# Performance work log

Hardware: AMD Instinct MI355X
Metric: run time of the kernel (lower is better)

## Reference

```python
import jax, jax.numpy as jnp
import numpy as np
from jax import lax

MAX_SCALE = 4
SCALES = [2 ** i for i in range(1, MAX_SCALE + 1)]  # [2, 4, 8, 16]
EPS = 1e-6
BN_EPS = 1e-3  # keras BatchNormalization default epsilon


def _box_sum(x, r):
    # DepthwiseConv2D with ones kernel, SAME zero padding == box sum window
    return lax.reduce_window(x, 0.0, lax.add, (1, r, r, 1), (1, 1, 1, 1), 'SAME')


def setup_inputs() -> dict:
    key = jax.random.key(0)
    k1, k2 = jax.random.split(key)
    B, H, W, C, K = 4, 224, 224, 64, 8
    return {
        'x': jax.random.normal(k1, (B, H, W, C), dtype=jnp.float32),
        'ols_weights': jnp.ones((MAX_SCALE,), jnp.float32),
        'anchors': jax.random.normal(k2, (C, K), dtype=jnp.float32),
        'hist_widths': jnp.ones((C, K), jnp.float32),
        'bn_gamma': jnp.ones((C,), jnp.float32),
        'bn_beta': jnp.zeros((C,), jnp.float32),
        'bn_mean': jnp.zeros((C,), jnp.float32),
        'bn_var': jnp.ones((C,), jnp.float32),
    }


def reference(x, ols_weights, anchors, hist_widths, bn_gamma, bn_beta, bn_mean, bn_var):
    # --- sample min-max scaling to [0, 1] per sample ---
    xmin = jnp.min(x, axis=(1, 2, 3), keepdims=True)
    xmax = jnp.max(x, axis=(1, 2, 3), keepdims=True)
    xs = (x - xmin) / (xmax - xmin + EPS)

    # --- multi-scale box measures: [B,H,W,C,S] ---
    measures = jnp.stack([_box_sum(xs, r) for r in SCALES], axis=-1)

    # --- weighted OLS slope of log(measure) vs log(scale) -> local alpha ---
    ly = jnp.log(measures + EPS)                         # [B,H,W,C,S]
    lr = jnp.log(jnp.asarray(SCALES, jnp.float32))       # [S]
    w = ols_weights                                       # [S]
    wsum = jnp.sum(w)
    lr_bar = jnp.sum(w * lr) / wsum
    ly_bar = jnp.sum(w * ly, axis=-1, keepdims=True) / wsum
    dx = lr - lr_bar                                      # [S]
    num = jnp.sum(w * dx * (ly - ly_bar), axis=-1)        # [B,H,W,C]
    den = jnp.sum(w * dx * dx)
    alphas = num / den

    # --- batch norm (inference mode, training=False) ---
    a = bn_gamma * (alphas - bn_mean) * lax.rsqrt(bn_var + BN_EPS) + bn_beta

    # --- triangular soft histogram over k anchors, relu'd and summed ---
    hist = 1.0 - hist_widths * jnp.abs(a[..., None] - anchors)  # [B,H,W,C,K]
    soft_counts = jnp.sum(jax.nn.relu(hist), axis=-1)           # [B,H,W,C]

    return x + jax.nn.sigmoid(soft_counts)
```

## Files before the change

kernel.cpp:

```cpp
#include <hip/hip_runtime.h>
#include <math.h>

#define B 4
#define H 224
#define W 224
#define C 64
#define K 8
#define WC (W*C)
#define HWC (H*W*C)

__device__ inline float wave_reduce_min(float v) {
  #pragma unroll
  for (int off = 32; off > 0; off >>= 1)
    v = fminf(v, __shfl_down(v, off, 64));
  return v;
}
__device__ inline float wave_reduce_max(float v) {
  #pragma unroll
  for (int off = 32; off > 0; off >>= 1)
    v = fmaxf(v, __shfl_down(v, off, 64));
  return v;
}

__global__ __launch_bounds__(256) void k_minmax_part(const float* __restrict__ x,
                                                     float* __restrict__ scratch) {
  int s   = blockIdx.x >> 9;
  int blk = blockIdx.x & 511;
  const float4* xs = (const float4*)(x + (size_t)s * HWC);
  const int n4 = HWC / 4;
  float vmin = INFINITY, vmax = -INFINITY;
  for (int i = blk*256 + threadIdx.x; i < n4; i += 512*256) {
    float4 v = xs[i];
    vmin = fminf(vmin, fminf(fminf(v.x, v.y), fminf(v.z, v.w)));
    vmax = fmaxf(vmax, fmaxf(fmaxf(v.x, v.y), fmaxf(v.z, v.w)));
  }
  __shared__ float smin[4], smax[4];
  float wmin = wave_reduce_min(vmin), wmax = wave_reduce_max(vmax);
  int wave = threadIdx.x >> 6, lane = threadIdx.x & 63;
  if (lane == 0) { smin[wave] = wmin; smax[wave] = wmax; }
  __syncthreads();
  if (threadIdx.x == 0) {
    float m = fminf(fminf(smin[0], smin[1]), fminf(smin[2], smin[3]));
    float M = fmaxf(fmaxf(smax[0], smax[1]), fmaxf(smax[2], smax[3]));
    scratch[blockIdx.x]        = m;
    scratch[2048 + blockIdx.x] = M;
  }
}

__global__ __launch_bounds__(256) void k_vpfx(const float* __restrict__ x,
                                              const float* __restrict__ scratch,
                                              float* __restrict__ P) {
  int bid = blockIdx.x;
  int b = bid / W, w = bid % W;
  int q = threadIdx.x >> 6, c = threadIdx.x & 63;

  float vmin = fminf(scratch[b*512 + threadIdx.x], scratch[b*512 + 256 + threadIdx.x] - 0.f);
  float vmax = fmaxf(scratch[2048 + b*512 + threadIdx.x], scratch[2048 + b*512 + 256 + threadIdx.x]);
  __shared__ float smin[4], smax[4];
  float wmin = wave_reduce_min(vmin), wmax = wave_reduce_max(vmax);
  if ((threadIdx.x & 63) == 0) { smin[q] = wmin; smax[q] = wmax; }
  __syncthreads();
  float xmin = fminf(fminf(smin[0], smin[1]), fminf(smin[2], smin[3]));
  float xmax = fmaxf(fmaxf(smax[0], smax[1]), fmaxf(smax[2], smax[3]));
  float inv  = 1.0f / (xmax - xmin + 1e-6f);

  size_t colbase = (size_t)b*HWC + (size_t)w*C + c;
  const int hq = q * 56;
  const float* xp = x + colbase + (size_t)hq * WC;

  float v[56];
  #pragma unroll
  for (int j = 0; j < 56; ++j) v[j] = xp[(size_t)j * WC];
  float sum = 0.f;
  #pragma unroll
  for (int j = 0; j < 56; ++j) sum += v[j];

  __shared__ float lds[256];
  lds[threadIdx.x] = sum;
  __syncthreads();

  float acc = 0.f;
  for (int qq = 0; qq < q; ++qq) acc += lds[qq*64 + c];

  float* Pp = P + colbase + (size_t)hq * WC;
  #pragma unroll
  for (int j = 0; j < 56; ++j) {
    acc += v[j];
    Pp[(size_t)j * WC] = (acc - (float)(hq + j + 1) * xmin) * inv;
  }
}

__global__ __launch_bounds__(128) void k_main(
    const float* __restrict__ P, const float* __restrict__ x,
    const float* __restrict__ ols, const float* __restrict__ anchors,
    const float* __restrict__ hwidths, const float* __restrict__ bn_gamma,
    const float* __restrict__ bn_beta, const float* __restrict__ bn_mean,
    const float* __restrict__ bn_var, float* __restrict__ out) {
  int xcd  = blockIdx.x & 7;
  int i    = blockIdx.x >> 3;
  int rg   = xcd * 112 + (i >> 2);
  int wave = threadIdx.x >> 6, c = threadIdx.x & 63;
  int chunk = (i & 3) * 2 + wave;
  int b = rg / H, h = rg % H;
  int w0 = chunk * 28;

  const float LN2 = 0.69314718055994530942f;
  float wg0 = ols[0], wg1 = ols[1], wg2 = ols[2], wg3 = ols[3];
  float l0 = LN2, l1 = 2.f*LN2, l2 = 3.f*LN2, l3 = 4.f*LN2;
  float wsum = wg0 + wg1 + wg2 + wg3;
  float lrbar = (wg0*l0 + wg1*l1 + wg2*l2 + wg3*l3) / wsum;
  float d0 = l0-lrbar, d1 = l1-lrbar, d2 = l2-lrbar, d3 = l3-lrbar;
  float den = wg0*d0*d0 + wg1*d1*d1 + wg2*d2*d2 + wg3*d3*d3;
  float c0 = wg0*d0/den, c1 = wg1*d1/den, c2 = wg2*d2/den, c3 = wg3*d3/den;

  float scl  = bn_gamma[c] * rsqrtf(bn_var[c] + 1e-3f);
  float bofs = bn_beta[c] - bn_mean[c] * scl;
  float anc[K], wd[K];
  #pragma unroll
  for (int k = 0; k < K; ++k) { anc[k] = anchors[c*K + k]; wd[k] = hwidths[c*K + k]; }

  const int hiA[4] = {1, 2, 4, 8};
  const int loA[4] = {0, 1, 3, 7};
  const float* pt[4]; const float* pb[4]; float fb[4];
  #pragma unroll
  for (int s = 0; s < 4; ++s) {
    int ht = h + hiA[s]; if (ht > H-1) ht = H-1;
    int hb = h - loA[s] - 1;
    int hbc = hb < 0 ? 0 : hb;
    pt[s] = P + (size_t)b*HWC + (size_t)ht*WC + c;
    pb[s] = P + (size_t)b*HWC + (size_t)hbc*WC + c;
    fb[s] = hb < 0 ? 0.f : 1.f;
  }

  const float* xrow = x   + (size_t)b*HWC + (size_t)h*WC + c;
  float*       orow = out + (size_t)b*HWC + (size_t)h*WC + c;

  float ring2[2]   = {0,0};
  float ring4[4]   = {0,0,0,0};
  float ring8[8]   = {0,0,0,0,0,0,0,0};
  float ring16[16] = {0,0,0,0,0,0,0,0,0,0,0,0,0,0,0,0};
  float T0 = 0.f, T1 = 0.f, T2 = 0.f, T3 = 0.f;
  float abuf[8] = {0,0,0,0,0,0,0,0};

  for (int t0 = 0; t0 < 48; t0 += 16) {
    #pragma unroll
    for (int u = 0; u < 16; ++u) {
      int t  = t0 + u;
      int wr = w0 - 7 + t;
      float m0 = 0.f, m1 = 0.f, m2 = 0.f, m3 = 0.f;
      if (wr >= 0 && wr < W) {
        int off = wr * C;
        m0 = pt[0][off] - fb[0]*pb[0][off];
        m1 = pt[1][off] - fb[1]*pb[1][off];
        m2 = pt[2][off] - fb[2]*pb[2][off];
        m3 = pt[3][off] - fb[3]*pb[3][off];
      }
      T0 += m0 - ring2[u&1];  ring2[u&1]  = m0;
      T1 += m1 - ring4[u&3];  ring4[u&3]  = m1;
      T2 += m2 - ring8[u&7];  ring8[u&7]  = m2;
      T3 += m3 - ring16[u];   ring16[u]   = m3;
      abuf[(u+7)&7] += c0 * __logf(fmaxf(T0, 0.f) + 1e-6f);
      abuf[(u+6)&7] += c1 * __logf(fmaxf(T1, 0.f) + 1e-6f);
      abuf[(u+4)&7] += c2 * __logf(fmaxf(T2, 0.f) + 1e-6f);
      abuf[u&7]     += c3 * __logf(fmaxf(T3, 0.f) + 1e-6f);
      int ig = w0 - 15 + t;
      if (t >= 15 && ig <= w0 + 27) {
        float alpha = abuf[u&7];
        float a = alpha * scl + bofs;
        float sc = 0.f;
        #pragma unroll
        for (int k = 0; k < K; ++k)
          sc += fmaxf(0.f, 1.f - wd[k]*fabsf(a - anc[k]));
        float sig = 1.f / (1.f + __expf(-sc));
        float xv = __builtin_nontemporal_load(&xrow[ig*C]);
        __builtin_nontemporal_store(xv + sig, &orow[ig*C]);
      }
      abuf[u&7] = 0.f;
    }
  }
}

extern "C" void kernel_launch(void* const* d_in, const int* in_sizes, int n_in,
                              void* d_out, int out_size, void* d_ws, size_t ws_size,
                              hipStream_t stream) {
  const float* x        = (const float*)d_in[0];
  const float* ols      = (const float*)d_in[1];
  const float* anchors  = (const float*)d_in[2];
  const float* hwidths  = (const float*)d_in[3];
  const float* bn_gamma = (const float*)d_in[4];
  const float* bn_beta  = (const float*)d_in[5];
  const float* bn_mean  = (const float*)d_in[6];
  const float* bn_var   = (const float*)d_in[7];
  float* out = (float*)d_out;
  float* P   = (float*)d_ws;
  float* scratch = out;

  hipLaunchKernelGGL(k_minmax_part, dim3(2048),  dim3(256), 0, stream, x, scratch);
  hipLaunchKernelGGL(k_vpfx,        dim3(B*W),   dim3(256), 0, stream, x, scratch, P);
  hipLaunchKernelGGL(k_main,        dim3(B*H*4), dim3(128), 0, stream,
                     P, x, ols, anchors, hwidths, bn_gamma, bn_beta, bn_mean, bn_var, out);
}
```

Before: 215.0 us.

## Fold min-max normalization into box sums and drop separate min-max pass

The prefix-sum kernel now stores raw column prefix sums and emits per-column min/max partials, which removes the standalone min-max reduction pass over x. The main kernel reduces those partials itself and applies the normalization algebraically: it subtracts count*xmin from the raw box sums and scales the epsilon by the range, since a log slope is invariant to a constant scale. Interior tiles get a specialized loop with no bounds checks and precomputed constants. The trade-off is an extra small reduction in every main-kernel block, plus a dependence on enough workspace for the partials, with a fallback to the old path otherwise.

```diff
diff --git a/kernel.cpp b/kernel.cpp
--- a/kernel.cpp
+++ b/kernel.cpp
@@ -21,6 +21,199 @@
     v = fmaxf(v, __shfl_down(v, off, 64));
   return v;
 }
+
+struct FalseT { static constexpr bool value = false; };
+struct TrueT  { static constexpr bool value = true; };
+
+
+__global__ __launch_bounds__(256) void k_vpfx_raw(const float* __restrict__ x,
+                                                  float* __restrict__ P,
+                                                  float* __restrict__ pmin,
+                                                  float* __restrict__ pmax) {
+  int bid = blockIdx.x;
+  int b = bid / W, w = bid % W;
+  int q = threadIdx.x >> 6, c = threadIdx.x & 63;
+  size_t colbase = (size_t)b*HWC + (size_t)w*C + c;
+  const int hq = q * 56;
+  const float* xp = x + colbase + (size_t)hq * WC;
+
+  float v[56];
+  #pragma unroll
+  for (int j = 0; j < 56; ++j) v[j] = xp[(size_t)j * WC];
+
+  float sum = 0.f, vmin = v[0], vmax = v[0];
+  #pragma unroll
+  for (int j = 0; j < 56; ++j) {
+    sum += v[j];
+    vmin = fminf(vmin, v[j]);
+    vmax = fmaxf(vmax, v[j]);
+  }
+
+  __shared__ float lds[256];
+  __shared__ float smin[4], smax[4];
+  lds[threadIdx.x] = sum;
+  float wmin = wave_reduce_min(vmin), wmax = wave_reduce_max(vmax);
+  if ((threadIdx.x & 63) == 0) { smin[q] = wmin; smax[q] = wmax; }
+  __syncthreads();
+  if (threadIdx.x == 0) {
+    pmin[bid] = fminf(fminf(smin[0], smin[1]), fminf(smin[2], smin[3]));
+    pmax[bid] = fmaxf(fmaxf(smax[0], smax[1]), fmaxf(smax[2], smax[3]));
+  }
+
+  float acc = 0.f;
+  for (int qq = 0; qq < q; ++qq) acc += lds[qq*64 + c];
+
+  float* Pp = P + colbase + (size_t)hq * WC;
+  #pragma unroll
+  for (int j = 0; j < 56; ++j) {
+    acc += v[j];
+    Pp[(size_t)j * WC] = acc;
+  }
+}
+
+__global__ __launch_bounds__(128) void k_main2(
+    const float* __restrict__ P, const float* __restrict__ x,
+    const float* __restrict__ pmin, const float* __restrict__ pmax,
+    const float* __restrict__ ols, const float* __restrict__ anchors,
+    const float* __restrict__ hwidths, const float* __restrict__ bn_gamma,
+    const float* __restrict__ bn_beta, const float* __restrict__ bn_mean,
+    const float* __restrict__ bn_var, float* __restrict__ out) {
+  int xcd  = blockIdx.x & 7;
+  int i    = blockIdx.x >> 3;
+  int rg   = xcd * 112 + (i >> 2);
+  int wave = threadIdx.x >> 6, c = threadIdx.x & 63;
+  int chunk = (i & 3) * 2 + wave;
+  int b = rg / H, h = rg % H;
+  int w0 = chunk * 28;
+
+  float vmin = INFINITY, vmax = -INFINITY;
+  for (int ii = threadIdx.x; ii < W; ii += 128) {
+    vmin = fminf(vmin, pmin[b*W + ii]);
+    vmax = fmaxf(vmax, pmax[b*W + ii]);
+  }
+  vmin = wave_reduce_min(vmin);
+  vmax = wave_reduce_max(vmax);
+  __shared__ float sred[4];
+  if ((threadIdx.x & 63) == 0) { sred[wave*2] = vmin; sred[wave*2+1] = vmax; }
+  __syncthreads();
+  float xmin = fminf(sred[0], sred[2]);
+  float xmax = fmaxf(sred[1], sred[3]);
+  float rng  = xmax - xmin + 1e-6f;
+  float epsp = 1e-6f * rng;
+
+  const float LN2 = 0.69314718055994530942f;
+  float wg0 = ols[0], wg1 = ols[1], wg2 = ols[2], wg3 = ols[3];
+  float l0 = LN2, l1 = 2.f*LN2, l2 = 3.f*LN2, l3 = 4.f*LN2;
+  float wsum = wg0 + wg1 + wg2 + wg3;
+  float lrbar = (wg0*l0 + wg1*l1 + wg2*l2 + wg3*l3) / wsum;
+  float d0 = l0-lrbar, d1 = l1-lrbar, d2 = l2-lrbar, d3 = l3-lrbar;
+  float den = wg0*d0*d0 + wg1*d1*d1 + wg2*d2*d2 + wg3*d3*d3;
+  float c0 = wg0*d0/den, c1 = wg1*d1/den, c2 = wg2*d2/den, c3 = wg3*d3/den;
+
+  float scl  = bn_gamma[c] * rsqrtf(bn_var[c] + 1e-3f);
+  float bofs = bn_beta[c] - bn_mean[c] * scl;
+  float anc[K], wd[K];
+  #pragma unroll
+  for (int k = 0; k < K; ++k) { anc[k] = anchors[c*K + k]; wd[k] = hwidths[c*K + k]; }
+
+  const int hiA[4] = {1, 2, 4, 8};
+  const int loA[4] = {0, 1, 3, 7};
+  const int rA[4]  = {2, 4, 8, 16};
+  const float* pt[4]; const float* pb[4]; float fb[4];
+  float Anh[4], Kin[4];
+  #pragma unroll
+  for (int s = 0; s < 4; ++s) {
+    int ht = h + hiA[s]; if (ht > H-1) ht = H-1;
+    int hb = h - loA[s] - 1;
+    int hbc = hb < 0 ? 0 : hb;
+    pt[s] = P + (size_t)b*HWC + (size_t)ht*WC + c;
+    pb[s] = P + (size_t)b*HWC + (size_t)hbc*WC + c;
+    fb[s] = hb < 0 ? 0.f : 1.f;
+    int h0 = h - loA[s]; if (h0 < 0) h0 = 0;
+    int nv = ht - h0 + 1;
+    Anh[s] = -(float)nv * xmin;
+    Kin[s] = (float)rA[s] * Anh[s] + epsp;
+  }
+
+  const float* xrow = x   + (size_t)b*HWC + (size_t)h*WC + c;
+  float*       orow = out + (size_t)b*HWC + (size_t)h*WC + c;
+
+  auto tloop = [&](auto EDGEC) {
+    constexpr bool EDGE = decltype(EDGEC)::value;
+    float ring2[2]   = {0,0};
+    float ring4[4]   = {0,0,0,0};
+    float ring8[8]   = {0,0,0,0,0,0,0,0};
+    float ring16[16] = {0,0,0,0,0,0,0,0,0,0,0,0,0,0,0,0};
+    float T0 = 0.f, T1 = 0.f, T2 = 0.f, T3 = 0.f;
+    float abuf[8] = {0,0,0,0,0,0,0,0};
+
+    for (int t0 = 0; t0 < 48; t0 += 16) {
+      #pragma unroll
+      for (int u = 0; u < 16; ++u) {
+        int t  = t0 + u;
+        int wr = w0 - 7 + t;
+        float m0, m1, m2, m3;
+        if constexpr (EDGE) {
+          m0 = m1 = m2 = m3 = 0.f;
+          if (wr >= 0 && wr < W) {
+            int off = wr * C;
+            m0 = pt[0][off] - fb[0]*pb[0][off];
+            m1 = pt[1][off] - fb[1]*pb[1][off];
+            m2 = pt[2][off] - fb[2]*pb[2][off];
+            m3 = pt[3][off] - fb[3]*pb[3][off];
+          }
+        } else {
+          int off = wr * C;
+          m0 = pt[0][off] - fb[0]*pb[0][off];
+          m1 = pt[1][off] - fb[1]*pb[1][off];
+          m2 = pt[2][off] - fb[2]*pb[2][off];
+          m3 = pt[3][off] - fb[3]*pb[3][off];
+        }
+        T0 += m0 - ring2[u&1];  ring2[u&1]  = m0;
+        T1 += m1 - ring4[u&3];  ring4[u&3]  = m1;
+        T2 += m2 - ring8[u&7];  ring8[u&7]  = m2;
+        T3 += m3 - ring16[u];   ring16[u]   = m3;
+
+        float a0, a1, a2, a3;
+        if constexpr (EDGE) {
+          float nh0 = (float)(min(wr, W-1) - max(wr-1,  0) + 1);
+          float nh1 = (float)(min(wr, W-1) - max(wr-3,  0) + 1);
+          float nh2 = (float)(min(wr, W-1) - max(wr-7,  0) + 1);
+          float nh3 = (float)(min(wr, W-1) - max(wr-15, 0) + 1);
+          a0 = fmaxf(fmaf(Anh[0], nh0, T0) + epsp, epsp);
+          a1 = fmaxf(fmaf(Anh[1], nh1, T1) + epsp, epsp);
+          a2 = fmaxf(fmaf(Anh[2], nh2, T2) + epsp, epsp);
+          a3 = fmaxf(fmaf(Anh[3], nh3, T3) + epsp, epsp);
+        } else {
+          a0 = fmaxf(T0 + Kin[0], epsp);
+          a1 = fmaxf(T1 + Kin[1], epsp);
+          a2 = fmaxf(T2 + Kin[2], epsp);
+          a3 = fmaxf(T3 + Kin[3], epsp);
+        }
+        abuf[(u+7)&7] += c0 * __logf(a0);
+        abuf[(u+6)&7] += c1 * __logf(a1);
+        abuf[(u+4)&7] += c2 * __logf(a2);
+        abuf[u&7]     += c3 * __logf(a3);
+
+        int ig = w0 - 15 + t;
+        if (t >= 15 && ig <= w0 + 27) {
+          float alpha = abuf[u&7];
+          float a = alpha * scl + bofs;
+          float sc = 0.f;
+          #pragma unroll
+          for (int k = 0; k < K; ++k)
+            sc += fmaxf(0.f, 1.f - wd[k]*fabsf(a - anc[k]));
+          float sig = 1.f / (1.f + __expf(-sc));
+          float xv = __builtin_nontemporal_load(&xrow[ig*C]);
+          __builtin_nontemporal_store(xv + sig, &orow[ig*C]);
+        }
+        abuf[u&7] = 0.f;
+      }
+    }
+  };
+  if (w0 >= 22 && w0 <= 183) tloop(FalseT{}); else tloop(TrueT{});
+}
+
 
 __global__ __launch_bounds__(256) void k_minmax_part(const float* __restrict__ x,
                                                      float* __restrict__ scratch) {
@@ -180,6 +373,7 @@
   }
 }
 
+
 extern "C" void kernel_launch(void* const* d_in, const int* in_sizes, int n_in,
                               void* d_out, int out_size, void* d_ws, size_t ws_size,
                               hipStream_t stream) {
@@ -193,10 +387,21 @@
   const float* bn_var   = (const float*)d_in[7];
   float* out = (float*)d_out;
   float* P   = (float*)d_ws;
-  float* scratch = out;
-
-  hipLaunchKernelGGL(k_minmax_part, dim3(2048),  dim3(256), 0, stream, x, scratch);
-  hipLaunchKernelGGL(k_vpfx,        dim3(B*W),   dim3(256), 0, stream, x, scratch, P);
-  hipLaunchKernelGGL(k_main,        dim3(B*H*4), dim3(128), 0, stream,
-                     P, x, ols, anchors, hwidths, bn_gamma, bn_beta, bn_mean, bn_var, out);
-}
+  const size_t PBYTES = (size_t)B * HWC * sizeof(float);
+
+  if (ws_size >= PBYTES + 8192) {
+    float* pmn = (float*)((char*)d_ws + PBYTES);
+    float* pmx = pmn + 1024;
+    hipLaunchKernelGGL(k_vpfx_raw, dim3(B*W),   dim3(256), 0, stream, x, P, pmn, pmx);
+    hipLaunchKernelGGL(k_main2,    dim3(B*H*4), dim3(128), 0, stream,
+                       P, x, pmn, pmx, ols, anchors, hwidths,
+                       bn_gamma, bn_beta, bn_mean, bn_var, out);
+  } else {
+    float* scratch = out;
+    hipLaunchKernelGGL(k_minmax_part, dim3(2048),  dim3(256), 0, stream, x, scratch);
+    hipLaunchKernelGGL(k_vpfx,        dim3(B*W),   dim3(256), 0, stream, x, scratch, P);
+    hipLaunchKernelGGL(k_main,        dim3(B*H*4), dim3(128), 0, stream,
+                       P, x, ols, anchors, hwidths,
+                       bn_gamma, bn_beta, bn_mean, bn_var, out);
+  }
+}
```

Result: slower. 227.4 us (+5.8%).

## Fuse min-max reduction into column prefix kernel using cooperative grid sync

Applied to the files above, without the earlier changes.

Replaces the separate min/max pass and the column prefix-sum kernel with one cooperative kernel. It loads each column once into registers with float4 vectors, computes the partial min/max and segment sums, then runs a grid-wide sync before normalising and writing P. This removes a full extra read of x and one kernel launch. The cost is a grid barrier, which needs all 896 blocks to be resident at once (launch bounds 256,4). If the cooperative launch fails or the workspace is too small, it falls back to the old three-kernel path.

```diff
diff --git a/kernel.cpp b/kernel.cpp
--- a/kernel.cpp
+++ b/kernel.cpp
@@ -1,4 +1,5 @@
 #include <hip/hip_runtime.h>
+#include <hip/hip_cooperative_groups.h>
 #include <math.h>
 
 #define B 4
@@ -9,6 +10,8 @@
 #define WC (W*C)
 #define HWC (H*W*C)
 
+namespace cg = cooperative_groups;
+
 __device__ inline float wave_reduce_min(float v) {
   #pragma unroll
   for (int off = 32; off > 0; off >>= 1)
@@ -22,71 +25,89 @@
   return v;
 }
 
-__global__ __launch_bounds__(256) void k_minmax_part(const float* __restrict__ x,
-                                                     float* __restrict__ scratch) {
-  int s   = blockIdx.x >> 9;
-  int blk = blockIdx.x & 511;
-  const float4* xs = (const float4*)(x + (size_t)s * HWC);
-  const int n4 = HWC / 4;
-  float vmin = INFINITY, vmax = -INFINITY;
-  for (int i = blk*256 + threadIdx.x; i < n4; i += 512*256) {
-    float4 v = xs[i];
-    vmin = fminf(vmin, fminf(fminf(v.x, v.y), fminf(v.z, v.w)));
-    vmax = fmaxf(vmax, fmaxf(fmaxf(v.x, v.y), fmaxf(v.z, v.w)));
-  }
-  __shared__ float smin[4], smax[4];
-  float wmin = wave_reduce_min(vmin), wmax = wave_reduce_max(vmax);
-  int wave = threadIdx.x >> 6, lane = threadIdx.x & 63;
-  if (lane == 0) { smin[wave] = wmin; smax[wave] = wmax; }
-  __syncthreads();
-  if (threadIdx.x == 0) {
-    float m = fminf(fminf(smin[0], smin[1]), fminf(smin[2], smin[3]));
-    float M = fmaxf(fmaxf(smax[0], smax[1]), fmaxf(smax[2], smax[3]));
-    scratch[blockIdx.x]        = m;
-    scratch[2048 + blockIdx.x] = M;
-  }
-}
-
-__global__ __launch_bounds__(256) void k_vpfx(const float* __restrict__ x,
-                                              const float* __restrict__ scratch,
-                                              float* __restrict__ P) {
+
+__global__ __launch_bounds__(256, 4) void k_vpfx_coop(const float* __restrict__ x,
+                                                      float* __restrict__ P,
+                                                      float* __restrict__ pmin,
+                                                      float* __restrict__ pmax) {
+  cg::grid_group grid = cg::this_grid();
+
   int bid = blockIdx.x;
   int b = bid / W, w = bid % W;
-  int q = threadIdx.x >> 6, c = threadIdx.x & 63;
-
-  float vmin = fminf(scratch[b*512 + threadIdx.x], scratch[b*512 + 256 + threadIdx.x] - 0.f);
-  float vmax = fmaxf(scratch[2048 + b*512 + threadIdx.x], scratch[2048 + b*512 + 256 + threadIdx.x]);
+  int seg = threadIdx.x >> 4;
+  int chg = threadIdx.x & 15;
+
+  const size_t colbase = (size_t)b*HWC + (size_t)w*C;
+  const float4* xp4 = (const float4*)(x + colbase);
+  const int RS4 = WC / 4;
+  const int r0 = seg * 14;
+
+  float4 v4[14];
+  #pragma unroll
+  for (int j = 0; j < 14; ++j) v4[j] = xp4[(size_t)(r0 + j) * RS4 + chg];
+
+  float4 s4 = v4[0];
+  float vmin = fminf(fminf(v4[0].x, v4[0].y), fminf(v4[0].z, v4[0].w));
+  float vmax = fmaxf(fmaxf(v4[0].x, v4[0].y), fmaxf(v4[0].z, v4[0].w));
+  #pragma unroll
+  for (int j = 1; j < 14; ++j) {
+    s4.x += v4[j].x; s4.y += v4[j].y; s4.z += v4[j].z; s4.w += v4[j].w;
+    vmin = fminf(vmin, fminf(fminf(v4[j].x, v4[j].y), fminf(v4[j].z, v4[j].w)));
+    vmax = fmaxf(vmax, fmaxf(fmaxf(v4[j].x, v4[j].y), fmaxf(v4[j].z, v4[j].w)));
+  }
+
+  __shared__ float4 segsum[16][16];
   __shared__ float smin[4], smax[4];
-  float wmin = wave_reduce_min(vmin), wmax = wave_reduce_max(vmax);
-  if ((threadIdx.x & 63) == 0) { smin[q] = wmin; smax[q] = wmax; }
+  segsum[seg][chg] = s4;
+  float wmn = wave_reduce_min(vmin), wmx = wave_reduce_max(vmax);
+  int wv = threadIdx.x >> 6;
+  if ((threadIdx.x & 63) == 0) { smin[wv] = wmn; smax[wv] = wmx; }
+  __syncthreads();
+
+  if (threadIdx.x == 0) {
+    pmin[bid] = fminf(fminf(smin[0], smin[1]), fminf(smin[2], smin[3]));
+    pmax[bid] = fmaxf(fmaxf(smax[0], smax[1]), fmaxf(smax[2], smax[3]));
+  }
+
+  float4 o4 = {0.f, 0.f, 0.f, 0.f};
+  #pragma unroll
+  for (int ss = 0; ss < 16; ++ss) {
+    if (ss < seg) {
+      float4 t = segsum[ss][chg];
+      o4.x += t.x; o4.y += t.y; o4.z += t.z; o4.w += t.w;
+    }
+  }
+
+  __threadfence();
+  grid.sync();
+
+  float fmn = INFINITY, fmx = -INFINITY;
+  for (int ii = b*W + (int)threadIdx.x; ii < b*W + W; ii += 256) {
+    fmn = fminf(fmn, pmin[ii]);
+    fmx = fmaxf(fmx, pmax[ii]);
+  }
+  fmn = wave_reduce_min(fmn);
+  fmx = wave_reduce_max(fmx);
+  __syncthreads();
+  if ((threadIdx.x & 63) == 0) { smin[wv] = fmn; smax[wv] = fmx; }
   __syncthreads();
   float xmin = fminf(fminf(smin[0], smin[1]), fminf(smin[2], smin[3]));
   float xmax = fmaxf(fmaxf(smax[0], smax[1]), fmaxf(smax[2], smax[3]));
   float inv  = 1.0f / (xmax - xmin + 1e-6f);
 
-  size_t colbase = (size_t)b*HWC + (size_t)w*C + c;
-  const int hq = q * 56;
-  const float* xp = x + colbase + (size_t)hq * WC;
-
-  float v[56];
-  #pragma unroll
-  for (int j = 0; j < 56; ++j) v[j] = xp[(size_t)j * WC];
-  float sum = 0.f;
-  #pragma unroll
-  for (int j = 0; j < 56; ++j) sum += v[j];
-
-  __shared__ float lds[256];
-  lds[threadIdx.x] = sum;
-  __syncthreads();
-
-  float acc = 0.f;
-  for (int qq = 0; qq < q; ++qq) acc += lds[qq*64 + c];
-
-  float* Pp = P + colbase + (size_t)hq * WC;
-  #pragma unroll
-  for (int j = 0; j < 56; ++j) {
-    acc += v[j];
-    Pp[(size_t)j * WC] = (acc - (float)(hq + j + 1) * xmin) * inv;
+  float4* Pp4 = (float4*)(P + colbase);
+  float ax = o4.x, ay = o4.y, az = o4.z, aw = o4.w;
+  #pragma unroll
+  for (int j = 0; j < 14; ++j) {
+    ax += v4[j].x; ay += v4[j].y; az += v4[j].z; aw += v4[j].w;
+    float cnt = (float)(r0 + j + 1);
+    float sub = cnt * xmin;
+    float4 outv;
+    outv.x = (ax - sub) * inv;
+    outv.y = (ay - sub) * inv;
+    outv.z = (az - sub) * inv;
+    outv.w = (aw - sub) * inv;
+    Pp4[(size_t)(r0 + j) * RS4 + chg] = outv;
   }
 }
 
@@ -180,6 +201,76 @@
   }
 }
 
+
+__global__ __launch_bounds__(256) void k_minmax_part(const float* __restrict__ x,
+                                                     float* __restrict__ scratch) {
+  int s   = blockIdx.x >> 9;
+  int blk = blockIdx.x & 511;
+  const float4* xs = (const float4*)(x + (size_t)s * HWC);
+  const int n4 = HWC / 4;
+  float vmin = INFINITY, vmax = -INFINITY;
+  for (int i = blk*256 + threadIdx.x; i < n4; i += 512*256) {
+    float4 v = xs[i];
+    vmin = fminf(vmin, fminf(fminf(v.x, v.y), fminf(v.z, v.w)));
+    vmax = fmaxf(vmax, fmaxf(fmaxf(v.x, v.y), fmaxf(v.z, v.w)));
+  }
+  __shared__ float smin[4], smax[4];
+  float wmin = wave_reduce_min(vmin), wmax = wave_reduce_max(vmax);
+  int wave = threadIdx.x >> 6, lane = threadIdx.x & 63;
+  if (lane == 0) { smin[wave] = wmin; smax[wave] = wmax; }
+  __syncthreads();
+  if (threadIdx.x == 0) {
+    float m = fminf(fminf(smin[0], smin[1]), fminf(smin[2], smin[3]));
+    float M = fmaxf(fmaxf(smax[0], smax[1]), fmaxf(smax[2], smax[3]));
+    scratch[blockIdx.x]        = m;
+    scratch[2048 + blockIdx.x] = M;
+  }
+}
+
+__global__ __launch_bounds__(256) void k_vpfx(const float* __restrict__ x,
+                                              const float* __restrict__ scratch,
+                                              float* __restrict__ P) {
+  int bid = blockIdx.x;
+  int b = bid / W, w = bid % W;
+  int q = threadIdx.x >> 6, c = threadIdx.x & 63;
+
+  float vmin = fminf(scratch[b*512 + threadIdx.x], scratch[b*512 + 256 + threadIdx.x] - 0.f);
+  float vmax = fmaxf(scratch[2048 + b*512 + threadIdx.x], scratch[2048 + b*512 + 256 + threadIdx.x]);
+  __shared__ float smin[4], smax[4];
+  float wmin = wave_reduce_min(vmin), wmax = wave_reduce_max(vmax);
+  if ((threadIdx.x & 63) == 0) { smin[q] = wmin; smax[q] = wmax; }
+  __syncthreads();
+  float xmin = fminf(fminf(smin[0], smin[1]), fminf(smin[2], smin[3]));
+  float xmax = fmaxf(fmaxf(smax[0], smax[1]), fmaxf(smax[2], smax[3]));
+  float inv  = 1.0f / (xmax - xmin + 1e-6f);
+
+  size_t colbase = (size_t)b*HWC + (size_t)w*C + c;
+  const int hq = q * 56;
+  const float* xp = x + colbase + (size_t)hq * WC;
+
+  float v[56];
+  #pragma unroll
+  for (int j = 0; j < 56; ++j) v[j] = xp[(size_t)j * WC];
+  float sum = 0.f;
+  #pragma unroll
+  for (int j = 0; j < 56; ++j) sum += v[j];
+
+  __shared__ float lds[256];
+  lds[threadIdx.x] = sum;
+  __syncthreads();
+
+  float acc = 0.f;
+  for (int qq = 0; qq < q; ++qq) acc += lds[qq*64 + c];
+
+  float* Pp = P + colbase + (size_t)hq * WC;
+  #pragma unroll
+  for (int j = 0; j < 56; ++j) {
+    acc += v[j];
+    Pp[(size_t)j * WC] = (acc - (float)(hq + j + 1) * xmin) * inv;
+  }
+}
+
+
 extern "C" void kernel_launch(void* const* d_in, const int* in_sizes, int n_in,
                               void* d_out, int out_size, void* d_ws, size_t ws_size,
                               hipStream_t stream) {
@@ -193,10 +284,29 @@
   const float* bn_var   = (const float*)d_in[7];
   float* out = (float*)d_out;
   float* P   = (float*)d_ws;
-  float* scratch = out;
-
-  hipLaunchKernelGGL(k_minmax_part, dim3(2048),  dim3(256), 0, stream, x, scratch);
-  hipLaunchKernelGGL(k_vpfx,        dim3(B*W),   dim3(256), 0, stream, x, scratch, P);
-  hipLaunchKernelGGL(k_main,        dim3(B*H*4), dim3(128), 0, stream,
-                     P, x, ols, anchors, hwidths, bn_gamma, bn_beta, bn_mean, bn_var, out);
-}
+  const size_t PBYTES = (size_t)B * HWC * sizeof(float);
+
+  bool done = false;
+  if (ws_size >= PBYTES + 8192) {
+    float* pmn = (float*)((char*)d_ws + PBYTES);
+    float* pmx = pmn + 1024;
+    void* args[] = { (void*)&x, (void*)&P, (void*)&pmn, (void*)&pmx };
+    hipError_t err = hipLaunchCooperativeKernel((const void*)k_vpfx_coop,
+                                                dim3(B*W), dim3(256),
+                                                args, 0, stream);
+    if (err == hipSuccess) {
+      hipLaunchKernelGGL(k_main, dim3(B*H*4), dim3(128), 0, stream,
+                         P, x, ols, anchors, hwidths,
+                         bn_gamma, bn_beta, bn_mean, bn_var, out);
+      done = true;
+    }
+  }
+  if (!done) {
+    float* scratch = out;
+    hipLaunchKernelGGL(k_minmax_part, dim3(2048),  dim3(256), 0, stream, x, scratch);
+    hipLaunchKernelGGL(k_vpfx,        dim3(B*W),   dim3(256), 0, stream, x, scratch, P);
+    hipLaunchKernelGGL(k_main,        dim3(B*H*4), dim3(128), 0, stream,
+                       P, x, ols, anchors, hwidths,
+                       bn_gamma, bn_beta, bn_mean, bn_var, out);
+  }
+}
```

Result: slower. 417.7 us (+94.3%).
